# Optimization experiments

Measured on AMD Instinct MI355X. Metric: run time of the kernel, lower is better.

Reference implementation:

```python
import jax, jax.numpy as jnp
import numpy as np

B, S, D = 2, 2048, 1024
H = 16
HD = D // H  # 64

def setup_inputs() -> dict:
    key = jax.random.key(0)
    ks = jax.random.split(key, 6)
    scale = 0.02
    x   = jax.random.normal(ks[0], (B, S, D), dtype=jnp.float32)
    Wq  = jax.random.normal(ks[1], (D, D), dtype=jnp.float32) * scale
    Wk  = jax.random.normal(ks[2], (D, D), dtype=jnp.float32) * scale
    Wv  = jax.random.normal(ks[3], (D, D), dtype=jnp.float32) * scale
    Wo  = jax.random.normal(ks[4], (D, D), dtype=jnp.float32) * scale
    bo  = jax.random.normal(ks[5], (D,), dtype=jnp.float32) * scale
    return {"x": x, "Wq": Wq, "Wk": Wk, "Wv": Wv, "Wo": Wo, "bo": bo}

def reference(x, Wq, Wk, Wv, Wo, bo):
    b, s, d = x.shape
    # QKV projections (no bias, qkv_bias=False); weights stored as [d_in, d_out]
    q = (x @ Wq).reshape(b, s, H, HD).transpose(0, 2, 1, 3)  # [b,h,s,hd]
    k = (x @ Wk).reshape(b, s, H, HD).transpose(0, 2, 1, 3)
    v = (x @ Wv).reshape(b, s, H, HD).transpose(0, 2, 1, 3)
    scores = jnp.einsum('bhqd,bhkd->bhqk', q, k)  # [b,h,s,s]
    causal = jnp.triu(jnp.ones((s, s), dtype=bool), k=1)
    scores = jnp.where(causal, -jnp.inf, scores)
    attn = jax.nn.softmax(scores / jnp.sqrt(jnp.float32(HD)), axis=-1)
    # dropout_rate = 0.0 -> identity
    ctx = jnp.einsum('bhqk,bhkd->bqhd', attn, v).reshape(b, s, d)
    return ctx @ Wo + bo
```

## Files before the change

kernel.cpp:

```cpp
#include <hip/hip_runtime.h>
#include <hip/hip_bf16.h>
#include <math.h>

#define B_ 2
#define S_ 2048
#define D_ 1024
#define H_ 16
#define HD_ 64
#define M_ (B_*S_)

typedef __attribute__((ext_vector_type(8))) short bf16x8;
typedef __attribute__((ext_vector_type(4))) float f32x4;

#define MFMA16(a,b,c) __builtin_amdgcn_mfma_f32_16x16x32_bf16(a,b,c,0,0,0)
#define INFF __builtin_inff()

static __device__ __forceinline__ unsigned short f2bf_bits(float f) {
    unsigned int u = __float_as_uint(f);
    unsigned int r = (u + 0x7fffu + ((u >> 16) & 1u)) >> 16;
    return (unsigned short)r;
}

static __device__ __forceinline__ void gload16(const unsigned short* g, unsigned short* l) {
    __builtin_amdgcn_global_load_lds(
        (const __attribute__((address_space(1))) unsigned int*)(g),
        (__attribute__((address_space(3))) unsigned int*)(l),
        16, 0, 0);
}

__global__ __launch_bounds__(256) void convert_x_kernel(
    const float* __restrict__ x, unsigned short* __restrict__ o) {
    size_t i = (size_t)blockIdx.x * 256 + threadIdx.x;
    float4 v = reinterpret_cast<const float4*>(x)[i];
    ushort4 u;
    u.x = f2bf_bits(v.x); u.y = f2bf_bits(v.y);
    u.z = f2bf_bits(v.z); u.w = f2bf_bits(v.w);
    reinterpret_cast<ushort4*>(o)[i] = u;
}

__global__ __launch_bounds__(256) void convw_kernel(
    const float* __restrict__ W0, const float* __restrict__ W1,
    const float* __restrict__ W2, const float* __restrict__ W3,
    unsigned short* __restrict__ OT) {
    __shared__ float t[32][33];
    const float* W = (blockIdx.z == 0) ? W0 : (blockIdx.z == 1) ? W1
                    : (blockIdx.z == 2) ? W2 : W3;
    unsigned short* O = OT + (size_t)blockIdx.z * D_ * D_;
    int tx = threadIdx.x & 31, ty = threadIdx.x >> 5;
    int kb = blockIdx.y * 32, nb = blockIdx.x * 32;
#pragma unroll
    for (int i = 0; i < 4; i++)
        t[ty + 8*i][tx] = W[(size_t)(kb + ty + 8*i) * D_ + nb + tx];
    __syncthreads();
#pragma unroll
    for (int i = 0; i < 4; i++) {
        int n = nb + ty + 8*i, k = kb + tx;
        O[(size_t)n * D_ + k] = f2bf_bits(t[tx][ty + 8*i]);
    }
}

template<int BN, int MODE>
__global__ __launch_bounds__(256) void gemm_gl(
    const unsigned short* __restrict__ A,
    const unsigned short* __restrict__ BT,
    void* __restrict__ outp,
    const float* __restrict__ bias)
{
    constexpr int K = 1024;
    constexpr int NF = (BN == 128) ? 4 : 2;
    __shared__ union {
        struct { unsigned short As[128][64]; unsigned short Bs[BN][64]; } g;
        unsigned short vt[(BN == 128) ? 128 : 1][136];
    } sm;
    const int m0 = blockIdx.x * 128;
    const int n0 = blockIdx.y * BN;
    const int tid = threadIdx.x, lane = tid & 63, wid = tid >> 6;
    const int wm = (wid >> 1) * 64;
    const int wn = (wid & 1) * (BN / 2);
    const int lrow = lane & 15, lk8 = lane >> 4, orow = lk8 * 4;
    f32x4 acc[4][NF] = {};

    for (int k0 = 0; k0 < K; k0 += 64) {
#pragma unroll
        for (int i = 0; i < 4; i++) {
            const int rbase = wid * 32 + i * 8;
            const int rl = rbase + (lane >> 3);
            const int sc = ((lane & 7) ^ (rl & 7)) << 3;
            gload16(A + (size_t)(m0 + rl) * K + k0 + sc, &sm.g.As[rbase][0]);
        }
#pragma unroll
        for (int i = 0; i < BN / 32; i++) {
            const int rbase = wid * (BN / 4) + i * 8;
            const int rl = rbase + (lane >> 3);
            const int sc = ((lane & 7) ^ (rl & 7)) << 3;
            gload16(BT + (size_t)(n0 + rl) * K + k0 + sc, &sm.g.Bs[rbase][0]);
        }
        __syncthreads();
#pragma unroll
        for (int ks = 0; ks < 2; ks++) {
            bf16x8 af[4], bfr[NF];
#pragma unroll
            for (int f = 0; f < 4; f++) {
                const int row = wm + f * 16 + lrow;
                const int p = (ks * 4 + lk8) ^ (row & 7);
                af[f] = *reinterpret_cast<const bf16x8*>(&sm.g.As[row][p * 8]);
            }
#pragma unroll
            for (int f = 0; f < NF; f++) {
                const int row = wn + f * 16 + lrow;
                const int p = (ks * 4 + lk8) ^ (row & 7);
                bfr[f] = *reinterpret_cast<const bf16x8*>(&sm.g.Bs[row][p * 8]);
            }
            __builtin_amdgcn_s_setprio(1);
#pragma unroll
            for (int mf = 0; mf < 4; mf++)
#pragma unroll
                for (int nf = 0; nf < NF; nf++)
                    acc[mf][nf] = MFMA16(af[mf], bfr[nf], acc[mf][nf]);
            __builtin_amdgcn_s_setprio(0);
        }
        __syncthreads();
    }

    if (MODE == 0) {
        const int which = n0 >> 10;
        const int nl0 = n0 & 1023;
        unsigned short* obase = (unsigned short*)outp + (size_t)which * 4194304;
        const float scale = (which == 0) ? 0.125f : 1.0f;
        if (which < 2) {
#pragma unroll
            for (int mf = 0; mf < 4; mf++)
#pragma unroll
                for (int nf = 0; nf < NF; nf++)
#pragma unroll
                    for (int r = 0; r < 4; r++) {
                        int m = m0 + wm + mf*16 + orow + r;
                        int n = nl0 + wn + nf*16 + lrow;
                        int b = m >> 11, s = m & 2047;
                        int h = n >> 6, hd = n & 63;
                        obase[(((size_t)(b*16 + h) * 2048 + s) << 6) + hd]
                            = f2bf_bits(acc[mf][nf][r] * scale);
                    }
        } else {
#pragma unroll
            for (int mf = 0; mf < 4; mf++)
#pragma unroll
                for (int nf = 0; nf < NF; nf++)
#pragma unroll
                    for (int r = 0; r < 4; r++)
                        sm.vt[wn + nf*16 + lrow][wm + mf*16 + orow + r] =
                            f2bf_bits(acc[mf][nf][r]);
            __syncthreads();
            const int n = tid >> 1, c0 = (tid & 1) * 64;
            const int ng = nl0 + n, h = ng >> 6, hd = ng & 63;
            const int b = m0 >> 11, sbase = (m0 & 2047) + c0;
            unsigned short* dst = obase +
                (((size_t)(b * 16 + h) * 64 + hd) * 2048 + sbase);
#pragma unroll
            for (int j = 0; j < 64; j += 8)
                *reinterpret_cast<bf16x8*>(dst + j) =
                    *reinterpret_cast<const bf16x8*>(&sm.vt[n][c0 + j]);
        }
    } else {
        float* o = (float*)outp;
#pragma unroll
        for (int mf = 0; mf < 4; mf++)
#pragma unroll
            for (int nf = 0; nf < NF; nf++)
#pragma unroll
                for (int r = 0; r < 4; r++) {
                    int m = m0 + wm + mf*16 + orow + r;
                    int n = n0 + wn + nf*16 + lrow;
                    o[(size_t)m * 1024 + n] = acc[mf][nf][r] + bias[n];
                }
    }
}

__global__ __launch_bounds__(256) void attn_kernel(
    const unsigned short* __restrict__ Q,
    const unsigned short* __restrict__ Kb,
    const unsigned short* __restrict__ VT,
    unsigned short* __restrict__ ctx)
{
    __shared__ unsigned short Ks[2][64][64];
    __shared__ unsigned short Vs[2][64][64];
    __shared__ unsigned short Pl[4][16][72];
    const int fid = blockIdx.x + 16 * blockIdx.y;
    const int xcd = fid & 7, t = fid >> 3;
    const int bh = xcd | ((t & 3) << 3);
    const int jp = t >> 2;
    const int lane = threadIdx.x & 63, wid = threadIdx.x >> 6;
    const int lrow = lane & 15, lk8 = lane >> 4, orow = lk8 * 4;
    const unsigned short* Qp = Q  + (size_t)bh * (S_ * 64);
    const unsigned short* Kp = Kb + (size_t)bh * (S_ * 64);
    const unsigned short* Vp = VT + (size_t)bh * (64 * S_);
    const int b = bh >> 4, h = bh & 15;

    auto stage = [&](int buf, int kv0) {
#pragma unroll
        for (int i = 0; i < 2; i++) {
            const int rbase = wid * 16 + 8 * i;
            const int rl = rbase + (lane >> 3);
            const int sc = (((lane & 7) ^ (rl & 7)) << 3);
            gload16(Kp + (size_t)(kv0 + rl) * 64 + sc, &Ks[buf][rbase][0]);
            gload16(Vp + (size_t)rl * S_ + kv0 + sc, &Vs[buf][rbase][0]);
        }
    };

#pragma unroll 1
    for (int half = 0; half < 2; half++) {
        const int qt = half ? (31 - jp) : jp;
        const int nb = qt + 1;
        const int q0 = qt * 64 + wid * 16;

        stage(0, 0);

        bf16x8 qf[2];
#pragma unroll
        for (int kt = 0; kt < 2; kt++)
            qf[kt] = *reinterpret_cast<const bf16x8*>(
                Qp + (size_t)(q0 + lrow) * 64 + kt*32 + lk8*8);

        f32x4 acc[4] = {};
        float lr[4] = {0.f, 0.f, 0.f, 0.f};

        __syncthreads();

#pragma unroll 1
        for (int kvb = 0; kvb < nb; kvb++) {
            const int cur = kvb & 1;
            if (kvb + 1 < nb) stage(cur ^ 1, (kvb + 1) * 64);

            f32x4 sacc[4] = {};
            __builtin_amdgcn_s_setprio(1);
#pragma unroll
            for (int kt = 0; kt < 2; kt++)
#pragma unroll
                for (int nf = 0; nf < 4; nf++) {
                    const int row = nf * 16 + lrow;
                    const int g = ((kt << 2) | lk8) ^ (row & 7);
                    bf16x8 kf = *reinterpret_cast<const bf16x8*>(&Ks[cur][row][g << 3]);
                    sacc[nf] = MFMA16(qf[kt], kf, sacc[nf]);
                }
            __builtin_amdgcn_s_setprio(0);
            if (kvb == qt) {
#pragma unroll
                for (int nf = 0; nf < 4; nf++)
#pragma unroll
                    for (int r = 0; r < 4; r++)
                        if (nf*16 + lrow > wid*16 + orow + r) sacc[nf][r] = -INFF;
            }
            float ps[4] = {0.f, 0.f, 0.f, 0.f};
#pragma unroll
            for (int nf = 0; nf < 4; nf++)
#pragma unroll
                for (int r = 0; r < 4; r++) {
                    float p = __expf(sacc[nf][r]);
                    sacc[nf][r] = p;
                    ps[r] += p;
                }
#pragma unroll
            for (int r = 0; r < 4; r++)
                lr[r] += ps[r];
#pragma unroll
            for (int nf = 0; nf < 4; nf++)
#pragma unroll
                for (int r = 0; r < 4; r++)
                    Pl[wid][orow + r][nf*16 + lrow] = f2bf_bits(sacc[nf][r]);
            bf16x8 pf[2];
#pragma unroll
            for (int kt = 0; kt < 2; kt++)
                pf[kt] = *reinterpret_cast<const bf16x8*>(&Pl[wid][lrow][kt*32 + lk8*8]);
            __builtin_amdgcn_s_setprio(1);
#pragma unroll
            for (int kt = 0; kt < 2; kt++)
#pragma unroll
                for (int nf = 0; nf < 4; nf++) {
                    const int row = nf * 16 + lrow;
                    const int g = ((kt << 2) | lk8) ^ (row & 7);
                    bf16x8 vf = *reinterpret_cast<const bf16x8*>(&Vs[cur][row][g << 3]);
                    acc[nf] = MFMA16(pf[kt], vf, acc[nf]);
                }
            __builtin_amdgcn_s_setprio(0);
            __syncthreads();
        }

#pragma unroll
        for (int d = 1; d < 16; d <<= 1)
#pragma unroll
            for (int r = 0; r < 4; r++)
                lr[r] += __shfl_xor(lr[r], d);
#pragma unroll
        for (int nf = 0; nf < 4; nf++)
#pragma unroll
            for (int r = 0; r < 4; r++) {
                int s = q0 + orow + r;
                int col = h * 64 + nf * 16 + lrow;
                ctx[((size_t)(b * S_ + s)) * D_ + col] = f2bf_bits(acc[nf][r] / lr[r]);
            }
    }
}

extern "C" void kernel_launch(void* const* d_in, const int* in_sizes, int n_in,
                              void* d_out, int out_size, void* d_ws, size_t ws_size,
                              hipStream_t stream) {
    const float* x  = (const float*)d_in[0];
    const float* Wq = (const float*)d_in[1];
    const float* Wk = (const float*)d_in[2];
    const float* Wv = (const float*)d_in[3];
    const float* Wo = (const float*)d_in[4];
    const float* bo = (const float*)d_in[5];
    float* out = (float*)d_out;

    char* ws = (char*)d_ws;
    unsigned short* xb  = (unsigned short*)(ws);
    unsigned short* WT  = (unsigned short*)(ws + 8388608);
    unsigned short* QKV = (unsigned short*)(ws + 16777216);
    unsigned short* ctx = (unsigned short*)(ws + 41943040);

    unsigned short* Qb  = QKV;
    unsigned short* Kb  = QKV + 4194304;
    unsigned short* VTb = QKV + 8388608;

    convert_x_kernel<<<dim3(4096), dim3(256), 0, stream>>>(x, xb);
    convw_kernel<<<dim3(32, 32, 4), dim3(256), 0, stream>>>(Wq, Wk, Wv, Wo, WT);

    gemm_gl<128, 0><<<dim3(32, 24), dim3(256), 0, stream>>>(
        xb, WT, (void*)QKV, (const float*)nullptr);

    attn_kernel<<<dim3(16, 32), dim3(256), 0, stream>>>(Qb, Kb, VTb, ctx);

    gemm_gl<64, 1><<<dim3(32, 16), dim3(256), 0, stream>>>(
        ctx, WT + 3145728, (void*)out, bo);
}
```

Measured before the change: 117.1 us.

## Split attention into one q-tile per block and transpose score MFMA

Each block used to process a mirrored pair of query tiles to balance causal work. Now each block handles a single query tile, with a 1D grid of twice as many blocks launched heaviest-tile-first, so the hardware scheduler does the load balancing. The QK^T MFMA operands are swapped so each lane holds scores for one query. That lets the row sum accumulate in a single register and lets P be written to LDS as packed 8-byte stores instead of scalar 2-byte stores. The final normalisation uses two cross-lane shuffles plus a broadcast shuffle. The cost is losing the explicit pairing balance and adding more block launches.

```diff
diff --git a/kernel.cpp b/kernel.cpp
--- a/kernel.cpp
+++ b/kernel.cpp
@@ -185,16 +185,18 @@
     __shared__ unsigned short Ks[2][64][64];
     __shared__ unsigned short Vs[2][64][64];
     __shared__ unsigned short Pl[4][16][72];
-    const int fid = blockIdx.x + 16 * blockIdx.y;
+    const int fid = blockIdx.x;
     const int xcd = fid & 7, t = fid >> 3;
     const int bh = xcd | ((t & 3) << 3);
-    const int jp = t >> 2;
+    const int qt = 31 - (t >> 2);
     const int lane = threadIdx.x & 63, wid = threadIdx.x >> 6;
     const int lrow = lane & 15, lk8 = lane >> 4, orow = lk8 * 4;
     const unsigned short* Qp = Q  + (size_t)bh * (S_ * 64);
     const unsigned short* Kp = Kb + (size_t)bh * (S_ * 64);
     const unsigned short* Vp = VT + (size_t)bh * (64 * S_);
     const int b = bh >> 4, h = bh & 15;
+    const int q0 = qt * 64 + wid * 16;
+    const int nb = qt + 1;
 
     auto stage = [&](int buf, int kv0) {
 #pragma unroll
@@ -207,97 +209,88 @@
         }
     };
 
+    stage(0, 0);
+
+    bf16x8 qf[2];
+#pragma unroll
+    for (int kt = 0; kt < 2; kt++)
+        qf[kt] = *reinterpret_cast<const bf16x8*>(
+            Qp + (size_t)(q0 + lrow) * 64 + kt*32 + lk8*8);
+
+    f32x4 acc[4] = {};
+    float lr = 0.f;
+
+    __syncthreads();
+
 #pragma unroll 1
-    for (int half = 0; half < 2; half++) {
-        const int qt = half ? (31 - jp) : jp;
-        const int nb = qt + 1;
-        const int q0 = qt * 64 + wid * 16;
-
-        stage(0, 0);
-
-        bf16x8 qf[2];
+    for (int kvb = 0; kvb < nb; kvb++) {
+        const int cur = kvb & 1;
+        if (kvb + 1 < nb) stage(cur ^ 1, (kvb + 1) * 64);
+
+        f32x4 sacc[4] = {};
+        __builtin_amdgcn_s_setprio(1);
 #pragma unroll
         for (int kt = 0; kt < 2; kt++)
-            qf[kt] = *reinterpret_cast<const bf16x8*>(
-                Qp + (size_t)(q0 + lrow) * 64 + kt*32 + lk8*8);
-
-        f32x4 acc[4] = {};
-        float lr[4] = {0.f, 0.f, 0.f, 0.f};
-
+#pragma unroll
+            for (int nf = 0; nf < 4; nf++) {
+                const int row = nf * 16 + lrow;
+                const int g = ((kt << 2) | lk8) ^ (row & 7);
+                bf16x8 kf = *reinterpret_cast<const bf16x8*>(&Ks[cur][row][g << 3]);
+                sacc[nf] = MFMA16(kf, qf[kt], sacc[nf]);
+            }
+        __builtin_amdgcn_s_setprio(0);
+        if (kvb == qt) {
+#pragma unroll
+            for (int nf = 0; nf < 4; nf++)
+#pragma unroll
+                for (int r = 0; r < 4; r++)
+                    if (nf*16 + orow + r > wid*16 + lrow) sacc[nf][r] = -INFF;
+        }
+#pragma unroll
+        for (int nf = 0; nf < 4; nf++)
+#pragma unroll
+            for (int r = 0; r < 4; r++) {
+                float p = __expf(sacc[nf][r]);
+                sacc[nf][r] = p;
+                lr += p;
+            }
+#pragma unroll
+        for (int nf = 0; nf < 4; nf++) {
+            uint2 w;
+            w.x = (unsigned)f2bf_bits(sacc[nf][0]) | ((unsigned)f2bf_bits(sacc[nf][1]) << 16);
+            w.y = (unsigned)f2bf_bits(sacc[nf][2]) | ((unsigned)f2bf_bits(sacc[nf][3]) << 16);
+            *reinterpret_cast<uint2*>(&Pl[wid][lrow][nf*16 + orow]) = w;
+        }
+        bf16x8 pf[2];
+#pragma unroll
+        for (int kt = 0; kt < 2; kt++)
+            pf[kt] = *reinterpret_cast<const bf16x8*>(&Pl[wid][lrow][kt*32 + lk8*8]);
+        __builtin_amdgcn_s_setprio(1);
+#pragma unroll
+        for (int kt = 0; kt < 2; kt++)
+#pragma unroll
+            for (int nf = 0; nf < 4; nf++) {
+                const int row = nf * 16 + lrow;
+                const int g = ((kt << 2) | lk8) ^ (row & 7);
+                bf16x8 vf = *reinterpret_cast<const bf16x8*>(&Vs[cur][row][g << 3]);
+                acc[nf] = MFMA16(pf[kt], vf, acc[nf]);
+            }
+        __builtin_amdgcn_s_setprio(0);
         __syncthreads();
-
-#pragma unroll 1
-        for (int kvb = 0; kvb < nb; kvb++) {
-            const int cur = kvb & 1;
-            if (kvb + 1 < nb) stage(cur ^ 1, (kvb + 1) * 64);
-
-            f32x4 sacc[4] = {};
-            __builtin_amdgcn_s_setprio(1);
-#pragma unroll
-            for (int kt = 0; kt < 2; kt++)
-#pragma unroll
-                for (int nf = 0; nf < 4; nf++) {
-                    const int row = nf * 16 + lrow;
-                    const int g = ((kt << 2) | lk8) ^ (row & 7);
-                    bf16x8 kf = *reinterpret_cast<const bf16x8*>(&Ks[cur][row][g << 3]);
-                    sacc[nf] = MFMA16(qf[kt], kf, sacc[nf]);
-                }
-            __builtin_amdgcn_s_setprio(0);
-            if (kvb == qt) {
-#pragma unroll
-                for (int nf = 0; nf < 4; nf++)
-#pragma unroll
-                    for (int r = 0; r < 4; r++)
-                        if (nf*16 + lrow > wid*16 + orow + r) sacc[nf][r] = -INFF;
-            }
-            float ps[4] = {0.f, 0.f, 0.f, 0.f};
-#pragma unroll
-            for (int nf = 0; nf < 4; nf++)
-#pragma unroll
-                for (int r = 0; r < 4; r++) {
-                    float p = __expf(sacc[nf][r]);
-                    sacc[nf][r] = p;
-                    ps[r] += p;
-                }
-#pragma unroll
-            for (int r = 0; r < 4; r++)
-                lr[r] += ps[r];
-#pragma unroll
-            for (int nf = 0; nf < 4; nf++)
-#pragma unroll
-                for (int r = 0; r < 4; r++)
-                    Pl[wid][orow + r][nf*16 + lrow] = f2bf_bits(sacc[nf][r]);
-            bf16x8 pf[2];
-#pragma unroll
-            for (int kt = 0; kt < 2; kt++)
-                pf[kt] = *reinterpret_cast<const bf16x8*>(&Pl[wid][lrow][kt*32 + lk8*8]);
-            __builtin_amdgcn_s_setprio(1);
-#pragma unroll
-            for (int kt = 0; kt < 2; kt++)
-#pragma unroll
-                for (int nf = 0; nf < 4; nf++) {
-                    const int row = nf * 16 + lrow;
-                    const int g = ((kt << 2) | lk8) ^ (row & 7);
-                    bf16x8 vf = *reinterpret_cast<const bf16x8*>(&Vs[cur][row][g << 3]);
-                    acc[nf] = MFMA16(pf[kt], vf, acc[nf]);
-                }
-            __builtin_amdgcn_s_setprio(0);
-            __syncthreads();
-        }
-
-#pragma unroll
-        for (int d = 1; d < 16; d <<= 1)
-#pragma unroll
-            for (int r = 0; r < 4; r++)
-                lr[r] += __shfl_xor(lr[r], d);
-#pragma unroll
-        for (int nf = 0; nf < 4; nf++)
-#pragma unroll
-            for (int r = 0; r < 4; r++) {
-                int s = q0 + orow + r;
-                int col = h * 64 + nf * 16 + lrow;
-                ctx[((size_t)(b * S_ + s)) * D_ + col] = f2bf_bits(acc[nf][r] / lr[r]);
-            }
+    }
+
+    lr += __shfl_xor(lr, 16);
+    lr += __shfl_xor(lr, 32);
+    const float inv = 1.0f / lr;
+#pragma unroll
+    for (int r = 0; r < 4; r++) {
+        const float linv = __shfl(inv, (lane & 48) + orow + r);
+#pragma unroll
+        for (int nf = 0; nf < 4; nf++) {
+            int s = q0 + orow + r;
+            int col = h * 64 + nf * 16 + lrow;
+            ctx[((size_t)(b * S_ + s)) * D_ + col] = f2bf_bits(acc[nf][r] * linv);
+        }
     }
 }
 
@@ -328,7 +321,7 @@
     gemm_gl<128, 0><<<dim3(32, 24), dim3(256), 0, stream>>>(
         xb, WT, (void*)QKV, (const float*)nullptr);
 
-    attn_kernel<<<dim3(16, 32), dim3(256), 0, stream>>>(Qb, Kb, VTb, ctx);
+    attn_kernel<<<dim3(1024), dim3(256), 0, stream>>>(Qb, Kb, VTb, ctx);
 
     gemm_gl<64, 1><<<dim3(32, 16), dim3(256), 0, stream>>>(
         ctx, WT + 3145728, (void*)out, bo);
```

New measurement: 112.6 us. -3.9%, faster.
